# Kernel optimization log

Hardware: AMD Instinct MI355X
Metric: run time of the kernel (lower is better)

## Reference

```python
import jax, jax.numpy as jnp
import numpy as np

D = 128
N_AUTHOR = 100000
N_PAPER = 200000
N_LAYERS = 2


def setup_inputs() -> dict:
    key = jax.random.key(0)
    ks = jax.random.split(key, 16)
    inp = {
        "x_author": jax.random.normal(ks[0], (N_AUTHOR, D), dtype=jnp.float32),
        "x_paper": jax.random.normal(ks[1], (N_PAPER, D), dtype=jnp.float32),
        "edge_index": jax.random.randint(ks[2], (2, 500000), 0, 100000, dtype=jnp.int32),
        "coauthor_edge_index": jax.random.randint(ks[3], (2, 250000), 0, 100000, dtype=jnp.int32),
        "supervision_edge_index": jax.random.randint(ks[4], (2, 100000), 0, 100000, dtype=jnp.int32),
    }
    scale = 1.0 / np.sqrt(D)
    names = ["W_a2p", "W_p2a", "W_aself", "W_pself", "W_co"]
    for i, n in enumerate(names):
        inp[n] = jax.random.uniform(ks[5 + i], (N_LAYERS, D, D), jnp.float32, -scale, scale)
        inp["b" + n[1:]] = jax.random.uniform(ks[10 + i], (N_LAYERS, D), jnp.float32, -scale, scale)
    return inp


def _linear(x, W, b):
    # torch.nn.Linear: y = x @ W.T + b
    return x @ W.T + b


def reference(x_author, x_paper, edge_index, coauthor_edge_index, supervision_edge_index,
              W_a2p, b_a2p, W_p2a, b_p2a, W_aself, b_aself, W_pself, b_pself, W_co, b_co):
    author_idx, paper_idx = edge_index[0], edge_index[1]
    co_src, co_dst = coauthor_edge_index[0], coauthor_edge_index[1]
    for l in range(N_LAYERS):
        # author -> paper messages
        msg_a = _linear(x_author[author_idx], W_a2p[l], b_a2p[l])       # [E, D]
        agg_to_papers = jax.ops.segment_sum(msg_a, paper_idx, num_segments=x_paper.shape[0])
        # paper -> author messages
        msg_p = _linear(x_paper[paper_idx], W_p2a[l], b_p2a[l])         # [E, D]
        agg_to_authors = jax.ops.segment_sum(msg_p, author_idx, num_segments=x_author.shape[0])
        x_paper = agg_to_papers + _linear(x_paper, W_pself[l], b_pself[l])
        x_author = agg_to_authors + _linear(x_author, W_aself[l], b_aself[l])
        # coauthor edges (author -> author)
        msg_co = _linear(x_author[co_src], W_co[l], b_co[l])            # [E_co, D]
        agg_co = jax.ops.segment_sum(msg_co, co_dst, num_segments=x_author.shape[0])
        x_author = x_author + agg_co
    a = x_author[supervision_edge_index[0]]
    p = x_paper[supervision_edge_index[1]]
    return (a * p).sum(axis=1)
```

## Files before the change

kernel.cpp:

```cpp
#include <hip/hip_runtime.h>

#define DD 128
#define ADJ_CAP 1024

typedef __attribute__((ext_vector_type(8))) short short8;
typedef __attribute__((ext_vector_type(4))) float f32x4;

__device__ inline unsigned short f2bf(float f) {
    unsigned u = __float_as_uint(f);
    unsigned r = (u + 0x7fffu + ((u >> 16) & 1u)) >> 16;
    return (unsigned short)r;
}
__device__ inline float bf2f(unsigned short u) {
    return __uint_as_float(((unsigned)u) << 16);
}
__device__ inline float bflo(unsigned u) { return __uint_as_float(u << 16); }
__device__ inline float bfhi(unsigned u) { return __uint_as_float(u & 0xffff0000u); }
__device__ inline unsigned pack2(float a, float b) {
    return (unsigned)f2bf(a) | ((unsigned)f2bf(b) << 16);
}

__global__ __launch_bounds__(256) void conv_all(const float* __restrict__ inA, unsigned short* __restrict__ outA, int n4A,
                                                const float* __restrict__ inP, unsigned short* __restrict__ outP, int n4P) {
    int i = blockIdx.x * blockDim.x + threadIdx.x;
    const float* in;
    unsigned short* out;
    int j;
    if (i < n4A) { in = inA; out = outA; j = i; }
    else if (i < n4A + n4P) { in = inP; out = outP; j = i - n4A; }
    else return;
    float4 v = *(const float4*)(in + (size_t)j * 4);
    uint2 o;
    o.x = pack2(v.x, v.y);
    o.y = pack2(v.z, v.w);
    *(uint2*)(out + (size_t)j * 4) = o;
}

__global__ __launch_bounds__(256) void pack_all(const float* __restrict__ Wa2p, const float* __restrict__ Wpself,
                                                const float* __restrict__ Wp2a, const float* __restrict__ Waself,
                                                const float* __restrict__ Wco,
                                                short* __restrict__ BPp0, short* __restrict__ BPp1,
                                                short* __restrict__ BPa0, short* __restrict__ BPa1,
                                                short* __restrict__ BPc0, short* __restrict__ BPc1) {
    const int WL = 128 * 128;
    int idx = blockIdx.x * blockDim.x + threadIdx.x;
    int seg = idx >> 12;
    int sidx = idx & 4095;
    const float *W1, *W2;
    short* dst;
    int ktiles;
    switch (seg) {
        case 0: W1 = Wa2p;      W2 = Wpself;      dst = BPp0; ktiles = 8; break;
        case 1: W1 = Wa2p + WL; W2 = Wpself + WL; dst = BPp1; ktiles = 8; break;
        case 2: W1 = Wp2a;      W2 = Waself;      dst = BPa0; ktiles = 8; break;
        case 3: W1 = Wp2a + WL; W2 = Waself + WL; dst = BPa1; ktiles = 8; break;
        case 4: W1 = Wco;       W2 = nullptr;     dst = BPc0; ktiles = 4; break;
        default: W1 = Wco + WL; W2 = nullptr;     dst = BPc1; ktiles = 4; break;
    }
    int total = 8 * ktiles * 64;
    if (sidx >= total) return;
    int lane = sidx & 63;
    int kk = (sidx >> 6) % ktiles;
    int t = (sidx >> 6) / ktiles;
    int n = t * 16 + (lane & 15);
    int kbase = kk * 32 + (lane >> 4) * 8;
    short8 v;
#pragma unroll
    for (int j = 0; j < 8; ++j) {
        int k = kbase + j;
        float f = (k < 128) ? W1[n * 128 + k] : W2[n * 128 + (k - 128)];
        v[j] = (short)f2bf(f);
    }
    *(short8*)(dst + (size_t)sidx * 8) = v;
}

__global__ __launch_bounds__(256) void count_all(const int* __restrict__ aidx, const int* __restrict__ pidx,
                                                 const int* __restrict__ cod,
                                                 int* __restrict__ cntP, int* __restrict__ cntA,
                                                 int* __restrict__ cntC, int E, int Eco) {
    int i = blockIdx.x * blockDim.x + threadIdx.x;
    if (i < E) {
        atomicAdd(&cntP[pidx[i]], 1);
        atomicAdd(&cntA[aidx[i]], 1);
    } else if (i < E + Eco) {
        atomicAdd(&cntC[cod[i - E]], 1);
    }
}

__global__ __launch_bounds__(256) void scan_local3(const int* __restrict__ c0, int* __restrict__ r0, int* __restrict__ p0, int N0,
                                                   const int* __restrict__ c1, int* __restrict__ r1, int* __restrict__ p1, int N1,
                                                   const int* __restrict__ c2, int* __restrict__ r2, int* __restrict__ p2, int N2,
                                                   int nb0, int nb1) {
    __shared__ int sh[256];
    int b = blockIdx.x;
    const int* cnt; int* row; int* partials; int N; int lb;
    if (b < nb0) { cnt = c0; row = r0; partials = p0; N = N0; lb = b; }
    else if (b < nb0 + nb1) { cnt = c1; row = r1; partials = p1; N = N1; lb = b - nb0; }
    else { cnt = c2; row = r2; partials = p2; N = N2; lb = b - nb0 - nb1; }
    int t = threadIdx.x;
    int base = lb * 1024 + t * 4;
    int v0 = 0, v1 = 0, v2 = 0, v3 = 0;
    if (base + 0 < N) v0 = cnt[base + 0];
    if (base + 1 < N) v1 = cnt[base + 1];
    if (base + 2 < N) v2 = cnt[base + 2];
    if (base + 3 < N) v3 = cnt[base + 3];
    sh[t] = v0 + v1 + v2 + v3;
    __syncthreads();
    for (int off = 1; off < 256; off <<= 1) {
        int y = (t >= off) ? sh[t - off] : 0;
        __syncthreads();
        sh[t] += y;
        __syncthreads();
    }
    int excl = (t > 0) ? sh[t - 1] : 0;
    if (t == 255) partials[lb] = sh[255];
    if (base + 0 < N) row[base + 0] = excl; excl += v0;
    if (base + 1 < N) row[base + 1] = excl; excl += v1;
    if (base + 2 < N) row[base + 2] = excl; excl += v2;
    if (base + 3 < N) row[base + 3] = excl;
}

__global__ __launch_bounds__(256) void scan_partials3(int* __restrict__ p0, int nb0,
                                                      int* __restrict__ p1, int nb1,
                                                      int* __restrict__ p2, int nb2) {
    __shared__ int sh[256];
    int* partials; int nb;
    if (blockIdx.x == 0) { partials = p0; nb = nb0; }
    else if (blockIdx.x == 1) { partials = p1; nb = nb1; }
    else { partials = p2; nb = nb2; }
    int t = threadIdx.x;
    int v = (t < nb) ? partials[t] : 0;
    sh[t] = v;
    __syncthreads();
    for (int off = 1; off < 256; off <<= 1) {
        int y = (t >= off) ? sh[t - off] : 0;
        __syncthreads();
        sh[t] += y;
        __syncthreads();
    }
    if (t < nb) partials[t] = (t > 0) ? sh[t - 1] : 0;
}

__global__ __launch_bounds__(256) void scan_finalize3(int* __restrict__ r0, int* __restrict__ cu0, const int* __restrict__ p0, int N0,
                                                      int* __restrict__ r1, int* __restrict__ cu1, const int* __restrict__ p1, int N1,
                                                      int* __restrict__ r2, int* __restrict__ cu2, const int* __restrict__ p2, int N2,
                                                      int fb0, int fb1) {
    int b = blockIdx.x;
    int* row; int* cur; const int* partials; int N; int lb;
    if (b < fb0) { row = r0; cur = cu0; partials = p0; N = N0; lb = b; }
    else if (b < fb0 + fb1) { row = r1; cur = cu1; partials = p1; N = N1; lb = b - fb0; }
    else { row = r2; cur = cu2; partials = p2; N = N2; lb = b - fb0 - fb1; }
    int i = lb * 256 + threadIdx.x;
    if (i >= N) return;
    int r = row[i] + partials[i >> 10];
    row[i] = r;
    cur[i] = r;
}

__global__ __launch_bounds__(256) void fill_all(const int* __restrict__ aidx, const int* __restrict__ pidx,
                                                const int* __restrict__ cos_, const int* __restrict__ cod,
                                                int* __restrict__ curP, int* __restrict__ curA, int* __restrict__ curC,
                                                int* __restrict__ adjP, int* __restrict__ adjA, int* __restrict__ adjC,
                                                int E, int Eco) {
    int i = blockIdx.x * blockDim.x + threadIdx.x;
    if (i < E) {
        int a = aidx[i], pp = pidx[i];
        adjP[atomicAdd(&curP[pp], 1)] = a;
        adjA[atomicAdd(&curA[a], 1)] = pp;
    } else if (i < E + Eco) {
        adjC[atomicAdd(&curC[cod[i - E]], 1)] = cos_[i - E];
    }
}

struct FParams {
    const unsigned short* gsrc;
    const unsigned short* selfx;
    const unsigned short* base;
    const int* adj;
    const int* rowp;
    const int* cnt;
    const short* Bpack;
    const float* b1;
    const float* b2;
    unsigned short* out;
    int M;
};

template <int KTILES, bool HAS_B2, bool ADD_BASE>
__device__ __forceinline__ void fused_body(char* lds, int* ldsAdj, const FParams& p, int blk) {
    const int tid = threadIdx.x;
    const int node0 = blk * 64;
    const int grp = tid >> 4;
    const int l = tid & 15;

    const int lastNode = (node0 + 63 < p.M) ? node0 + 63 : p.M - 1;
    const int est = p.rowp[node0];
    const int eend = p.rowp[lastNode] + p.cnt[lastNode];
    const int nE = eend - est;
    for (int j = tid; j < nE && j < ADJ_CAP; j += 256) ldsAdj[j] = p.adj[est + j];

    int relSt[4], dA[4];
#pragma unroll
    for (int i = 0; i < 4; ++i) {
        int node = node0 + grp * 4 + i;
        bool ok = node < p.M;
        relSt[i] = ok ? (p.rowp[node] - est) : 0;
        dA[i] = ok ? p.cnt[node] : 0;
    }
    __syncthreads();

    float acc[4][8];
#pragma unroll
    for (int i = 0; i < 4; ++i)
#pragma unroll
        for (int j = 0; j < 8; ++j) acc[i][j] = 0.f;

    int dmax = dA[0];
#pragma unroll
    for (int i = 1; i < 4; ++i) dmax = dA[i] > dmax ? dA[i] : dmax;

    for (int k = 0; k < dmax; k += 2) {
#pragma unroll
        for (int i = 0; i < 4; ++i) {
            if (k < dA[i]) {
                int rem = dA[i] - k;
                int o0 = relSt[i] + k;
                int o1 = o0 + ((rem > 1) ? 1 : 0);
                int s0 = (o0 < ADJ_CAP) ? ldsAdj[o0] : p.adj[est + o0];
                int s1 = (o1 < ADJ_CAP) ? ldsAdj[o1] : p.adj[est + o1];
                float w1 = (rem > 1) ? 1.f : 0.f;
                uint4 v0 = *(const uint4*)(p.gsrc + (size_t)s0 * DD + l * 8);
                uint4 v1 = *(const uint4*)(p.gsrc + (size_t)s1 * DD + l * 8);
                acc[i][0] += bflo(v0.x); acc[i][1] += bfhi(v0.x);
                acc[i][2] += bflo(v0.y); acc[i][3] += bfhi(v0.y);
                acc[i][4] += bflo(v0.z); acc[i][5] += bfhi(v0.z);
                acc[i][6] += bflo(v0.w); acc[i][7] += bfhi(v0.w);
                acc[i][0] += w1 * bflo(v1.x); acc[i][1] += w1 * bfhi(v1.x);
                acc[i][2] += w1 * bflo(v1.y); acc[i][3] += w1 * bfhi(v1.y);
                acc[i][4] += w1 * bflo(v1.z); acc[i][5] += w1 * bfhi(v1.z);
                acc[i][6] += w1 * bflo(v1.w); acc[i][7] += w1 * bfhi(v1.w);
            }
        }
    }

#pragma unroll
    for (int i = 0; i < 4; ++i) {
        int lr = grp * 4 + i;
        uint4 o = make_uint4(pack2(acc[i][0], acc[i][1]), pack2(acc[i][2], acc[i][3]),
                             pack2(acc[i][4], acc[i][5]), pack2(acc[i][6], acc[i][7]));
        int colb = l * 16;
        *(uint4*)(lds + lr * 256 + (colb ^ ((lr & 7) << 4))) = o;
    }
    __syncthreads();

    const int wave = tid >> 6;
    const int lane = tid & 63;
    const int kg = lane >> 4;
    const int lrA = wave * 16 + (lane & 15);

    f32x4 facc[8];
#pragma unroll
    for (int t = 0; t < 8; ++t) facc[t] = (f32x4){0.f, 0.f, 0.f, 0.f};

#pragma unroll
    for (int kk = 0; kk < 4; ++kk) {
        int colb = kk * 64 + kg * 16;
        short8 af = *(const short8*)(lds + lrA * 256 + (colb ^ ((lrA & 7) << 4)));
#pragma unroll
        for (int t = 0; t < 8; ++t) {
            short8 bf = *(const short8*)(p.Bpack + ((size_t)(t * KTILES + kk) * 64 + lane) * 8);
            facc[t] = __builtin_amdgcn_mfma_f32_16x16x32_bf16(af, bf, facc[t], 0, 0, 0);
        }
    }
    if (KTILES == 8) {
        int srow = node0 + wave * 16 + (lane & 15);
        if (srow >= p.M) srow = p.M - 1;
        const unsigned short* sp = p.selfx + (size_t)srow * DD + kg * 8;
#pragma unroll
        for (int kk = 4; kk < 8; ++kk) {
            short8 af = *(const short8*)(sp + (kk - 4) * 32);
#pragma unroll
            for (int t = 0; t < 8; ++t) {
                short8 bf = *(const short8*)(p.Bpack + ((size_t)(t * 8 + kk) * 64 + lane) * 8);
                facc[t] = __builtin_amdgcn_mfma_f32_16x16x32_bf16(af, bf, facc[t], 0, 0, 0);
            }
        }
    }

    const int col0 = lane & 15;
    const int crow0 = node0 + wave * 16 + kg * 4;
#pragma unroll
    for (int t = 0; t < 8; ++t) {
        int col = t * 16 + col0;
        float bb = p.b1[col];
        float b2v = HAS_B2 ? p.b2[col] : 0.f;
#pragma unroll
        for (int r = 0; r < 4; ++r) {
            int row = crow0 + r;
            if (row < p.M) {
                float v = facc[t][r] + (float)p.cnt[row] * bb + b2v;
                if (ADD_BASE) v += bf2f(p.base[(size_t)row * DD + col]);
                p.out[(size_t)row * DD + col] = f2bf(v);
            }
        }
    }
}

__global__ __launch_bounds__(256, 8) void fused_dual_kernel(FParams pP, FParams pA, int blkP) {
    __shared__ char lds[16384];
    __shared__ int ldsAdj[ADJ_CAP];
    bool isP = (int)blockIdx.x < blkP;
    const FParams& p = isP ? pP : pA;
    fused_body<8, true, false>(lds, ldsAdj, p, isP ? blockIdx.x : blockIdx.x - blkP);
}

__global__ __launch_bounds__(256, 8) void fused_co_kernel(FParams p) {
    __shared__ char lds[16384];
    __shared__ int ldsAdj[ADJ_CAP];
    fused_body<4, false, true>(lds, ldsAdj, p, blockIdx.x);
}

__global__ __launch_bounds__(256) void dot_kernel(
    const unsigned short* __restrict__ xa, const unsigned short* __restrict__ xp,
    const int* __restrict__ s0, const int* __restrict__ s1,
    float* __restrict__ out, int E) {
    int g = blockIdx.x * blockDim.x + threadIdx.x;
    int e = g >> 4;
    int l = g & 15;
    if (e >= E) return;
    int a = s0[e], p = s1[e];
    uint4 va = *(const uint4*)(xa + (size_t)a * DD + l * 8);
    uint4 vp = *(const uint4*)(xp + (size_t)p * DD + l * 8);
    float s = bflo(va.x) * bflo(vp.x) + bfhi(va.x) * bfhi(vp.x)
            + bflo(va.y) * bflo(vp.y) + bfhi(va.y) * bfhi(vp.y)
            + bflo(va.z) * bflo(vp.z) + bfhi(va.z) * bfhi(vp.z)
            + bflo(va.w) * bflo(vp.w) + bfhi(va.w) * bfhi(vp.w);
    s += __shfl_xor(s, 1); s += __shfl_xor(s, 2);
    s += __shfl_xor(s, 4); s += __shfl_xor(s, 8);
    if (l == 0) out[e] = s;
}

extern "C" void kernel_launch(void* const* d_in, const int* in_sizes, int n_in,
                              void* d_out, int out_size, void* d_ws, size_t ws_size,
                              hipStream_t stream) {
    const float* xa_in = (const float*)d_in[0];
    const float* xp_in = (const float*)d_in[1];
    const int* eidx = (const int*)d_in[2];
    const int* co = (const int*)d_in[3];
    const int* sup = (const int*)d_in[4];
    const float* W_a2p = (const float*)d_in[5];
    const float* b_a2p = (const float*)d_in[6];
    const float* W_p2a = (const float*)d_in[7];
    const float* b_p2a = (const float*)d_in[8];
    const float* W_aself = (const float*)d_in[9];
    const float* b_aself = (const float*)d_in[10];
    const float* W_pself = (const float*)d_in[11];
    const float* b_pself = (const float*)d_in[12];
    const float* W_co = (const float*)d_in[13];
    const float* b_co = (const float*)d_in[14];

    const int NA = in_sizes[0] / DD;
    const int NP = in_sizes[1] / DD;
    const int E = in_sizes[2] / 2;
    const int Eco = in_sizes[3] / 2;
    const int Esup = in_sizes[4] / 2;
    const int* a_idx = eidx;
    const int* p_idx = eidx + E;
    const int* co_s = co;
    const int* co_d = co + Eco;
    const int* s0 = sup;
    const int* s1 = sup + Esup;

    char* w = (char*)d_ws;
    auto carve = [&](size_t bytes) -> char* {
        char* p = w;
        w += (bytes + 255) & ~(size_t)255;
        return p;
    };
    unsigned short* XA = (unsigned short*)carve((size_t)NA * DD * 2);
    unsigned short* XP = (unsigned short*)carve((size_t)NP * DD * 2);
    unsigned short* P0b = (unsigned short*)carve((size_t)NP * DD * 2);
    unsigned short* P1b = (unsigned short*)carve((size_t)NP * DD * 2);
    unsigned short* A0b = (unsigned short*)carve((size_t)NA * DD * 2);
    unsigned short* A1b = (unsigned short*)carve((size_t)NA * DD * 2);
    int* cntP = (int*)carve((size_t)NP * 4);
    int* cntA = (int*)carve((size_t)NA * 4);
    int* cntC = (int*)carve((size_t)NA * 4);
    size_t cntSpan = (size_t)((char*)cntC - (char*)cntP) + (((size_t)NA * 4 + 255) & ~(size_t)255);
    int* rowP = (int*)carve((size_t)NP * 4);
    int* curP = (int*)carve((size_t)NP * 4);
    int* rowA = (int*)carve((size_t)NA * 4);
    int* curA = (int*)carve((size_t)NA * 4);
    int* rowC = (int*)carve((size_t)NA * 4);
    int* curC = (int*)carve((size_t)NA * 4);
    int* adjP = (int*)carve((size_t)E * 4);
    int* adjA = (int*)carve((size_t)E * 4);
    int* adjC = (int*)carve((size_t)Eco * 4);
    int* partP = (int*)carve(256 * 4);
    int* partA = (int*)carve(256 * 4);
    int* partC = (int*)carve(256 * 4);
    short* BPp0 = (short*)carve(8 * 8 * 64 * 8 * 2);
    short* BPp1 = (short*)carve(8 * 8 * 64 * 8 * 2);
    short* BPa0 = (short*)carve(8 * 8 * 64 * 8 * 2);
    short* BPa1 = (short*)carve(8 * 8 * 64 * 8 * 2);
    short* BPc0 = (short*)carve(8 * 4 * 64 * 8 * 2);
    short* BPc1 = (short*)carve(8 * 4 * 64 * 8 * 2);

    int n4A = NA * DD / 4, n4P = NP * DD / 4;
    conv_all<<<(n4A + n4P + 255) / 256, 256, 0, stream>>>(xa_in, XA, n4A, xp_in, XP, n4P);
    pack_all<<<96, 256, 0, stream>>>(W_a2p, W_pself, W_p2a, W_aself, W_co, BPp0, BPp1, BPa0, BPa1, BPc0, BPc1);

    hipMemsetAsync(cntP, 0, cntSpan, stream);
    count_all<<<(E + Eco + 255) / 256, 256, 0, stream>>>(a_idx, p_idx, co_d, cntP, cntA, cntC, E, Eco);
    const int nbP = (NP + 1023) / 1024;
    const int nbA = (NA + 1023) / 1024;
    scan_local3<<<nbP + nbA + nbA, 256, 0, stream>>>(cntP, rowP, partP, NP, cntA, rowA, partA, NA, cntC, rowC, partC, NA, nbP, nbA);
    scan_partials3<<<3, 256, 0, stream>>>(partP, nbP, partA, nbA, partC, nbA);
    const int fbP = (NP + 255) / 256;
    const int fbA = (NA + 255) / 256;
    scan_finalize3<<<fbP + fbA + fbA, 256, 0, stream>>>(rowP, curP, partP, NP, rowA, curA, partA, NA, rowC, curC, partC, NA, fbP, fbA);
    fill_all<<<(E + Eco + 255) / 256, 256, 0, stream>>>(a_idx, p_idx, co_s, co_d, curP, curA, curC, adjP, adjA, adjC, E, Eco);

    const int blkP = (NP + 63) / 64;
    const int blkA = (NA + 63) / 64;

    FParams pP1 = {XA, XP, nullptr, adjP, rowP, cntP, BPp0, b_a2p, b_pself, P0b, NP};
    FParams pA1 = {XP, XA, nullptr, adjA, rowA, cntA, BPa0, b_p2a, b_aself, A0b, NA};
    FParams pC1 = {A0b, nullptr, A0b, adjC, rowC, cntC, BPc0, b_co, nullptr, A1b, NA};
    FParams pP2 = {A1b, P0b, nullptr, adjP, rowP, cntP, BPp1, b_a2p + 128, b_pself + 128, P1b, NP};
    FParams pA2 = {P0b, A1b, nullptr, adjA, rowA, cntA, BPa1, b_p2a + 128, b_aself + 128, A0b, NA};
    FParams pC2 = {A0b, nullptr, A0b, adjC, rowC, cntC, BPc1, b_co + 128, nullptr, A1b, NA};

    fused_dual_kernel<<<blkP + blkA, 256, 0, stream>>>(pP1, pA1, blkP);
    fused_co_kernel<<<blkA, 256, 0, stream>>>(pC1);
    fused_dual_kernel<<<blkP + blkA, 256, 0, stream>>>(pP2, pA2, blkP);
    fused_co_kernel<<<blkA, 256, 0, stream>>>(pC2);

    dot_kernel<<<(Esup * 16 + 255) / 256, 256, 0, stream>>>(A1b, P1b, s0, s1, (float*)d_out, Esup);
}
```

Measured before the change: 619.2 us.

## Stage neighbor rows into LDS per wave with double-buffered async global_load_lds

The neighbor-gather aggregation is restructured so each wave handles its own 16 nodes. It stages the wave's adjacency list in LDS, then streams source feature rows into a per-wave double-buffered LDS window using global_load_lds, waiting on vmcnt to overlap the next chunk's loads with accumulation of the current one. The aim is to hide gather latency better than the old per-thread direct global loads. In exchange, LDS per block roughly doubles and launch bounds drop from 8 to 4 blocks per CU, which cuts occupancy. Waves with more than 256 edges fall back to a plain per-node loop.

```diff
diff --git a/kernel.cpp b/kernel.cpp
--- a/kernel.cpp
+++ b/kernel.cpp
@@ -1,7 +1,8 @@
 #include <hip/hip_runtime.h>
 
 #define DD 128
-#define ADJ_CAP 1024
+#define ADJW 256
+#define CHW 8
 
 typedef __attribute__((ext_vector_type(8))) short short8;
 typedef __attribute__((ext_vector_type(4))) float f32x4;
@@ -187,27 +188,32 @@
 };
 
 template <int KTILES, bool HAS_B2, bool ADD_BASE>
-__device__ __forceinline__ void fused_body(char* lds, int* ldsAdj, const FParams& p, int blk) {
+__device__ __forceinline__ void fused_body(char* ldsAgg, char* xwin, int* adjW, const FParams& p, int blk) {
     const int tid = threadIdx.x;
     const int node0 = blk * 64;
+    const int wave = tid >> 6;
+    const int lane = tid & 63;
+    const int grpw = lane >> 4;
+    const int l16 = lane & 15;
     const int grp = tid >> 4;
-    const int l = tid & 15;
-
-    const int lastNode = (node0 + 63 < p.M) ? node0 + 63 : p.M - 1;
-    const int est = p.rowp[node0];
-    const int eend = p.rowp[lastNode] + p.cnt[lastNode];
-    const int nE = eend - est;
-    for (int j = tid; j < nE && j < ADJ_CAP; j += 256) ldsAdj[j] = p.adj[est + j];
+
+    const int wrow0 = node0 + wave * 16;
+    int wst = 0, wend = 0;
+    if (wrow0 < p.M) {
+        int rlast = wrow0 + 15 < p.M ? wrow0 + 15 : p.M - 1;
+        wst = p.rowp[wrow0];
+        wend = p.rowp[rlast] + p.cnt[rlast];
+    }
+    const int nEw = wend - wst;
 
     int relSt[4], dA[4];
 #pragma unroll
     for (int i = 0; i < 4; ++i) {
-        int node = node0 + grp * 4 + i;
+        int node = wrow0 + grpw * 4 + i;
         bool ok = node < p.M;
-        relSt[i] = ok ? (p.rowp[node] - est) : 0;
+        relSt[i] = ok ? (p.rowp[node] - wst) : 0;
         dA[i] = ok ? p.cnt[node] : 0;
     }
-    __syncthreads();
 
     float acc[4][8];
 #pragma unroll
@@ -215,30 +221,63 @@
 #pragma unroll
         for (int j = 0; j < 8; ++j) acc[i][j] = 0.f;
 
-    int dmax = dA[0];
-#pragma unroll
-    for (int i = 1; i < 4; ++i) dmax = dA[i] > dmax ? dA[i] : dmax;
-
-    for (int k = 0; k < dmax; k += 2) {
+    char* xw = xwin + wave * 4096;
+    int* aw = adjW + wave * ADJW;
+
+    if (nEw > 0 && nEw <= ADJW) {
+        for (int j = lane; j < nEw; j += 64) aw[j] = p.adj[wst + j];
+
+        const int nW = (nEw + CHW - 1) / CHW;
+
+        auto issueW = [&](int w, int buf) {
+            int e0 = w * CHW;
+#pragma unroll
+            for (int q = 0; q < 2; ++q) {
+                int e = e0 + q * 4 + grpw;
+                if (e >= nEw) e = nEw - 1;
+                int src = aw[e];
+                const char* g = (const char*)(p.gsrc + (size_t)src * DD) + l16 * 16;
+                char* dst = xw + buf * 2048 + q * 1024;
+                __builtin_amdgcn_global_load_lds((const unsigned int*)g, (unsigned int*)dst, 16, 0, 0);
+            }
+        };
+
+        issueW(0, 0);
+        if (nW > 1) issueW(1, 1);
+
+        for (int w = 0; w < nW; ++w) {
+            if (w + 1 < nW) { asm volatile("s_waitcnt vmcnt(2)" ::: "memory"); }
+            else            { asm volatile("s_waitcnt vmcnt(0)" ::: "memory"); }
+            __builtin_amdgcn_sched_barrier(0);
+            const char* xb = xw + (w & 1) * 2048;
+            const int base = w * CHW;
+            const int wcap = (base + CHW < nEw) ? base + CHW : nEw;
+#pragma unroll
+            for (int i = 0; i < 4; ++i) {
+                int lo = relSt[i] > base ? relSt[i] : base;
+                int hi = relSt[i] + dA[i];
+                if (hi > wcap) hi = wcap;
+                for (int o = lo; o < hi; ++o) {
+                    uint4 v = *(const uint4*)(xb + (o - base) * 256 + l16 * 16);
+                    acc[i][0] += bflo(v.x); acc[i][1] += bfhi(v.x);
+                    acc[i][2] += bflo(v.y); acc[i][3] += bfhi(v.y);
+                    acc[i][4] += bflo(v.z); acc[i][5] += bfhi(v.z);
+                    acc[i][6] += bflo(v.w); acc[i][7] += bfhi(v.w);
+                }
+            }
+            __builtin_amdgcn_sched_barrier(0);
+            if (w + 2 < nW) issueW(w + 2, w & 1);
+        }
+    } else if (nEw > 0) {
 #pragma unroll
         for (int i = 0; i < 4; ++i) {
-            if (k < dA[i]) {
-                int rem = dA[i] - k;
-                int o0 = relSt[i] + k;
-                int o1 = o0 + ((rem > 1) ? 1 : 0);
-                int s0 = (o0 < ADJ_CAP) ? ldsAdj[o0] : p.adj[est + o0];
-                int s1 = (o1 < ADJ_CAP) ? ldsAdj[o1] : p.adj[est + o1];
-                float w1 = (rem > 1) ? 1.f : 0.f;
-                uint4 v0 = *(const uint4*)(p.gsrc + (size_t)s0 * DD + l * 8);
-                uint4 v1 = *(const uint4*)(p.gsrc + (size_t)s1 * DD + l * 8);
-                acc[i][0] += bflo(v0.x); acc[i][1] += bfhi(v0.x);
-                acc[i][2] += bflo(v0.y); acc[i][3] += bfhi(v0.y);
-                acc[i][4] += bflo(v0.z); acc[i][5] += bfhi(v0.z);
-                acc[i][6] += bflo(v0.w); acc[i][7] += bfhi(v0.w);
-                acc[i][0] += w1 * bflo(v1.x); acc[i][1] += w1 * bfhi(v1.x);
-                acc[i][2] += w1 * bflo(v1.y); acc[i][3] += w1 * bfhi(v1.y);
-                acc[i][4] += w1 * bflo(v1.z); acc[i][5] += w1 * bfhi(v1.z);
-                acc[i][6] += w1 * bflo(v1.w); acc[i][7] += w1 * bfhi(v1.w);
+            for (int k = 0; k < dA[i]; ++k) {
+                int src = p.adj[wst + relSt[i] + k];
+                uint4 v = *(const uint4*)((const char*)(p.gsrc + (size_t)src * DD) + l16 * 16);
+                acc[i][0] += bflo(v.x); acc[i][1] += bfhi(v.x);
+                acc[i][2] += bflo(v.y); acc[i][3] += bfhi(v.y);
+                acc[i][4] += bflo(v.z); acc[i][5] += bfhi(v.z);
+                acc[i][6] += bflo(v.w); acc[i][7] += bfhi(v.w);
             }
         }
     }
@@ -248,13 +287,11 @@
         int lr = grp * 4 + i;
         uint4 o = make_uint4(pack2(acc[i][0], acc[i][1]), pack2(acc[i][2], acc[i][3]),
                              pack2(acc[i][4], acc[i][5]), pack2(acc[i][6], acc[i][7]));
-        int colb = l * 16;
-        *(uint4*)(lds + lr * 256 + (colb ^ ((lr & 7) << 4))) = o;
+        int colb = l16 * 16;
+        *(uint4*)(ldsAgg + lr * 256 + (colb ^ ((lr & 7) << 4))) = o;
     }
     __syncthreads();
 
-    const int wave = tid >> 6;
-    const int lane = tid & 63;
     const int kg = lane >> 4;
     const int lrA = wave * 16 + (lane & 15);
 
@@ -265,7 +302,7 @@
 #pragma unroll
     for (int kk = 0; kk < 4; ++kk) {
         int colb = kk * 64 + kg * 16;
-        short8 af = *(const short8*)(lds + lrA * 256 + (colb ^ ((lrA & 7) << 4)));
+        short8 af = *(const short8*)(ldsAgg + lrA * 256 + (colb ^ ((lrA & 7) << 4)));
 #pragma unroll
         for (int t = 0; t < 8; ++t) {
             short8 bf = *(const short8*)(p.Bpack + ((size_t)(t * KTILES + kk) * 64 + lane) * 8);
@@ -306,18 +343,20 @@
     }
 }
 
-__global__ __launch_bounds__(256, 8) void fused_dual_kernel(FParams pP, FParams pA, int blkP) {
-    __shared__ char lds[16384];
-    __shared__ int ldsAdj[ADJ_CAP];
+__global__ __launch_bounds__(256, 4) void fused_dual_kernel(FParams pP, FParams pA, int blkP) {
+    __shared__ char ldsAgg[16384];
+    __shared__ char xwin[16384];
+    __shared__ int adjW[4 * ADJW];
     bool isP = (int)blockIdx.x < blkP;
     const FParams& p = isP ? pP : pA;
-    fused_body<8, true, false>(lds, ldsAdj, p, isP ? blockIdx.x : blockIdx.x - blkP);
-}
-
-__global__ __launch_bounds__(256, 8) void fused_co_kernel(FParams p) {
-    __shared__ char lds[16384];
-    __shared__ int ldsAdj[ADJ_CAP];
-    fused_body<4, false, true>(lds, ldsAdj, p, blockIdx.x);
+    fused_body<8, true, false>(ldsAgg, xwin, adjW, p, isP ? blockIdx.x : blockIdx.x - blkP);
+}
+
+__global__ __launch_bounds__(256, 4) void fused_co_kernel(FParams p) {
+    __shared__ char ldsAgg[16384];
+    __shared__ char xwin[16384];
+    __shared__ int adjW[4 * ADJW];
+    fused_body<4, false, true>(ldsAgg, xwin, adjW, p, blockIdx.x);
 }
 
 __global__ __launch_bounds__(256) void dot_kernel(
```

After: 557.7 us. -9.9%, faster.

## Stage self features through LDS and specialize gather on adjacency location

Applied to the files above, without the earlier changes.

The self-feature rows are now prefetched with coalesced loads at kernel start and written into LDS next to the aggregated rows. The MFMA loop then reads all K tiles from LDS and no longer does a strided per-lane global read of selfx inside the matrix loop. The gather loop is specialized by whether the whole adjacency fits in LDS, which removes the per-edge branch. In exchange the LDS footprint doubles to 32 KB and the launch-bound occupancy hints drop, so fewer blocks may be resident per CU.

```diff
diff --git a/kernel.cpp b/kernel.cpp
--- a/kernel.cpp
+++ b/kernel.cpp
@@ -188,6 +188,7 @@
 
 template <int KTILES, bool HAS_B2, bool ADD_BASE>
 __device__ __forceinline__ void fused_body(char* lds, int* ldsAdj, const FParams& p, int blk) {
+    constexpr int STRB = KTILES * 64;
     const int tid = threadIdx.x;
     const int node0 = blk * 64;
     const int grp = tid >> 4;
@@ -199,6 +200,16 @@
     const int nE = eend - est;
     for (int j = tid; j < nE && j < ADJ_CAP; j += 256) ldsAdj[j] = p.adj[est + j];
 
+    uint4 selfv[4];
+    if (KTILES == 8) {
+#pragma unroll
+        for (int i = 0; i < 4; ++i) {
+            int node = node0 + grp * 4 + i;
+            if (node >= p.M) node = p.M - 1;
+            selfv[i] = *(const uint4*)(p.selfx + (size_t)node * DD + l * 8);
+        }
+    }
+
     int relSt[4], dA[4];
 #pragma unroll
     for (int i = 0; i < 4; ++i) {
@@ -219,29 +230,32 @@
 #pragma unroll
     for (int i = 1; i < 4; ++i) dmax = dA[i] > dmax ? dA[i] : dmax;
 
-    for (int k = 0; k < dmax; k += 2) {
-#pragma unroll
-        for (int i = 0; i < 4; ++i) {
-            if (k < dA[i]) {
-                int rem = dA[i] - k;
-                int o0 = relSt[i] + k;
-                int o1 = o0 + ((rem > 1) ? 1 : 0);
-                int s0 = (o0 < ADJ_CAP) ? ldsAdj[o0] : p.adj[est + o0];
-                int s1 = (o1 < ADJ_CAP) ? ldsAdj[o1] : p.adj[est + o1];
-                float w1 = (rem > 1) ? 1.f : 0.f;
-                uint4 v0 = *(const uint4*)(p.gsrc + (size_t)s0 * DD + l * 8);
-                uint4 v1 = *(const uint4*)(p.gsrc + (size_t)s1 * DD + l * 8);
-                acc[i][0] += bflo(v0.x); acc[i][1] += bfhi(v0.x);
-                acc[i][2] += bflo(v0.y); acc[i][3] += bfhi(v0.y);
-                acc[i][4] += bflo(v0.z); acc[i][5] += bfhi(v0.z);
-                acc[i][6] += bflo(v0.w); acc[i][7] += bfhi(v0.w);
-                acc[i][0] += w1 * bflo(v1.x); acc[i][1] += w1 * bfhi(v1.x);
-                acc[i][2] += w1 * bflo(v1.y); acc[i][3] += w1 * bfhi(v1.y);
-                acc[i][4] += w1 * bflo(v1.z); acc[i][5] += w1 * bfhi(v1.z);
-                acc[i][6] += w1 * bflo(v1.w); acc[i][7] += w1 * bfhi(v1.w);
+    auto gather = [&](auto idxAt) {
+        for (int k = 0; k < dmax; k += 2) {
+#pragma unroll
+            for (int i = 0; i < 4; ++i) {
+                if (k < dA[i]) {
+                    int rem = dA[i] - k;
+                    int o0 = relSt[i] + k;
+                    int s0 = idxAt(o0);
+                    int s1 = idxAt(o0 + ((rem > 1) ? 1 : 0));
+                    float w1 = (rem > 1) ? 1.f : 0.f;
+                    uint4 v0 = *(const uint4*)(p.gsrc + (size_t)s0 * DD + l * 8);
+                    uint4 v1 = *(const uint4*)(p.gsrc + (size_t)s1 * DD + l * 8);
+                    acc[i][0] += bflo(v0.x); acc[i][1] += bfhi(v0.x);
+                    acc[i][2] += bflo(v0.y); acc[i][3] += bfhi(v0.y);
+                    acc[i][4] += bflo(v0.z); acc[i][5] += bfhi(v0.z);
+                    acc[i][6] += bflo(v0.w); acc[i][7] += bfhi(v0.w);
+                    acc[i][0] += w1 * bflo(v1.x); acc[i][1] += w1 * bfhi(v1.x);
+                    acc[i][2] += w1 * bflo(v1.y); acc[i][3] += w1 * bfhi(v1.y);
+                    acc[i][4] += w1 * bflo(v1.z); acc[i][5] += w1 * bfhi(v1.z);
+                    acc[i][6] += w1 * bflo(v1.w); acc[i][7] += w1 * bfhi(v1.w);
+                }
             }
         }
-    }
+    };
+    if (nE <= ADJ_CAP) gather([&](int o) { return ldsAdj[o]; });
+    else               gather([&](int o) { return p.adj[est + o]; });
 
 #pragma unroll
     for (int i = 0; i < 4; ++i) {
@@ -249,7 +263,15 @@
         uint4 o = make_uint4(pack2(acc[i][0], acc[i][1]), pack2(acc[i][2], acc[i][3]),
                              pack2(acc[i][4], acc[i][5]), pack2(acc[i][6], acc[i][7]));
         int colb = l * 16;
-        *(uint4*)(lds + lr * 256 + (colb ^ ((lr & 7) << 4))) = o;
+        *(uint4*)(lds + lr * STRB + (colb ^ ((lr & 7) << 4))) = o;
+    }
+    if (KTILES == 8) {
+#pragma unroll
+        for (int i = 0; i < 4; ++i) {
+            int lr = grp * 4 + i;
+            int colb = 256 + l * 16;
+            *(uint4*)(lds + lr * STRB + (colb ^ ((lr & 7) << 4))) = selfv[i];
+        }
     }
     __syncthreads();
 
@@ -263,27 +285,13 @@
     for (int t = 0; t < 8; ++t) facc[t] = (f32x4){0.f, 0.f, 0.f, 0.f};
 
 #pragma unroll
-    for (int kk = 0; kk < 4; ++kk) {
+    for (int kk = 0; kk < KTILES; ++kk) {
         int colb = kk * 64 + kg * 16;
-        short8 af = *(const short8*)(lds + lrA * 256 + (colb ^ ((lrA & 7) << 4)));
+        short8 af = *(const short8*)(lds + lrA * STRB + (colb ^ ((lrA & 7) << 4)));
 #pragma unroll
         for (int t = 0; t < 8; ++t) {
             short8 bf = *(const short8*)(p.Bpack + ((size_t)(t * KTILES + kk) * 64 + lane) * 8);
             facc[t] = __builtin_amdgcn_mfma_f32_16x16x32_bf16(af, bf, facc[t], 0, 0, 0);
-        }
-    }
-    if (KTILES == 8) {
-        int srow = node0 + wave * 16 + (lane & 15);
-        if (srow >= p.M) srow = p.M - 1;
-        const unsigned short* sp = p.selfx + (size_t)srow * DD + kg * 8;
-#pragma unroll
-        for (int kk = 4; kk < 8; ++kk) {
-            short8 af = *(const short8*)(sp + (kk - 4) * 32);
-#pragma unroll
-            for (int t = 0; t < 8; ++t) {
-                short8 bf = *(const short8*)(p.Bpack + ((size_t)(t * 8 + kk) * 64 + lane) * 8);
-                facc[t] = __builtin_amdgcn_mfma_f32_16x16x32_bf16(af, bf, facc[t], 0, 0, 0);
-            }
         }
     }
 
@@ -306,15 +314,15 @@
     }
 }
 
-__global__ __launch_bounds__(256, 8) void fused_dual_kernel(FParams pP, FParams pA, int blkP) {
-    __shared__ char lds[16384];
+__global__ __launch_bounds__(256, 4) void fused_dual_kernel(FParams pP, FParams pA, int blkP) {
+    __shared__ char lds[32768];
     __shared__ int ldsAdj[ADJ_CAP];
     bool isP = (int)blockIdx.x < blkP;
     const FParams& p = isP ? pP : pA;
     fused_body<8, true, false>(lds, ldsAdj, p, isP ? blockIdx.x : blockIdx.x - blkP);
 }
 
-__global__ __launch_bounds__(256, 8) void fused_co_kernel(FParams p) {
+__global__ __launch_bounds__(256, 6) void fused_co_kernel(FParams p) {
     __shared__ char lds[16384];
     __shared__ int ldsAdj[ADJ_CAP];
     fused_body<4, false, true>(lds, ldsAdj, p, blockIdx.x);
```

New measurement: 572.4 us. 1.08x faster.
